# Kernel optimization log

Hardware: AMD Instinct MI355X
Metric: run time of the kernel (lower is better)

Reference implementation:

```python
import jax, jax.numpy as jnp
import numpy as np

B, D_IN, H, A, L, HEADS, C = 1024, 512, 768, 5001, 4, 2, 2
N_DATA = 56000.0
NEG = -1e30


def _gru_step(x, h, Wih, Whh, bih, bhh):
    # torch nn.GRU gate order: r, z, n
    gi = x @ Wih + bih            # [B, 3H]
    gh = h @ Whh + bhh            # [B, 3H]
    i_r, i_z, i_n = jnp.split(gi, 3, axis=-1)
    h_r, h_z, h_n = jnp.split(gh, 3, axis=-1)
    r = jax.nn.sigmoid(i_r + h_r)
    z = jax.nn.sigmoid(i_z + h_z)
    n = jnp.tanh(i_n + r * h_n)
    return (1.0 - z) * n + z * h


def _atom_selector(cls, mask, Wih, Whh, bih, bhh, hW, hb, ae_w, key):
    # cls: [B, H]; mask: [B, A] int32 (mutable copy); dropout in eval mode (identity)
    h = jnp.zeros_like(cls)
    cur_in = cls
    ae_const = jax.lax.stop_gradient(ae_w)
    probs = []
    max_index = None
    rows = jnp.arange(B)
    for j in range(L):
        h = _gru_step(cur_in, h, Wih, Whh, bih, bhh)
        logits = h @ hW + hb                      # [B, A]
        if j == 0:
            col0 = jnp.where(mask.sum(axis=-1) == 0, 1, mask[:, 0])
            mask = mask.at[:, 0].set(col0)
        else:
            mask = jnp.where((max_index == 0)[:, None], 0, mask)
            mask = mask.at[:, 0].set(1)
        masked = jnp.where(mask > 0, logits, NEG)
        u = jax.random.uniform(jax.random.fold_in(key, j), (B, A), minval=1e-9, maxval=1.0)
        g = -jnp.log(-jnp.log(u))
        y_soft = jax.nn.softmax(masked + g, axis=-1)  # tau = 1
        ind = jnp.argmax(y_soft, axis=-1)             # [B]
        y_hard = jax.nn.one_hot(ind, A, dtype=y_soft.dtype)
        prob = y_hard + y_soft - jax.lax.stop_gradient(y_soft)  # straight-through
        mask = mask.at[rows, ind].set(0)              # scatter-zero chosen atoms
        probs.append(prob)
        max_index = ind
        cur_in = cls + prob @ ae_const                # atom embedding feedback
    return jnp.stack(probs, axis=1)                   # [B, L, A]


def reference(x, x_mask, W1, b1, W2, b2, W3, b3, gru_Wih, gru_Whh, gru_bih, gru_bhh,
              head_W, head_b, ae_w, ce_Wmu, ce_bmu, ce_Wcov, ce_bcov, alpha):
    # linear_base MLP
    h = jax.nn.relu(x @ W1 + b1)
    h = jax.nn.relu(h @ W2 + b2)
    h = h @ W3 + b3                                   # cls embedding [B, H]
    key = jax.random.key(42)
    atom_probs, cps = [], []
    for i in range(HEADS):
        ap = _atom_selector(h, x_mask, gru_Wih[i], gru_Whh[i], gru_bih[i], gru_bhh[i],
                            head_W[i], head_b[i], ae_w, jax.random.fold_in(key, i))
        atom_probs.append(ap)
        # consequent estimator stand-in: mu [B,C], coverage [B]
        pooled = ap.mean(axis=1)                      # [B, A]
        mu = jax.nn.sigmoid(pooled @ ce_Wmu + ce_bmu)
        coverage = jax.nn.sigmoid(pooled @ ce_Wcov + ce_bcov)
        n = coverage * N_DATA
        sf = (alpha[0] / n)[:, None]                  # [B, 1] -> broadcast to [B, C]
        cp = (mu + sf) / (1.0 + 2.0 * sf)
        cps.append(cp)
    mat_cp = jnp.stack(cps, axis=1)                   # [B, HEADS, C]
    out = jnp.log(mat_cp.mean(axis=1))                # [B, C]
    return out, jnp.stack(atom_probs, axis=1), mat_cp


def setup_inputs() -> dict:
    key = jax.random.key(0)
    ks = jax.random.split(key, 16)
    s = 0.02
    nrm = lambda k, sh: jax.random.normal(k, sh, dtype=jnp.float32) * s
    return {
        'x': jax.random.normal(ks[0], (B, D_IN), dtype=jnp.float32),
        'x_mask': jax.random.randint(ks[1], (B, A), 0, 2, dtype=jnp.int32),
        'W1': nrm(ks[2], (D_IN, H)), 'b1': jnp.zeros((H,), jnp.float32),
        'W2': nrm(ks[3], (H, H)), 'b2': jnp.zeros((H,), jnp.float32),
        'W3': nrm(ks[4], (H, H)), 'b3': jnp.zeros((H,), jnp.float32),
        'gru_Wih': nrm(ks[5], (HEADS, H, 3 * H)), 'gru_Whh': nrm(ks[6], (HEADS, H, 3 * H)),
        'gru_bih': jnp.zeros((HEADS, 3 * H), jnp.float32), 'gru_bhh': jnp.zeros((HEADS, 3 * H), jnp.float32),
        'head_W': nrm(ks[7], (HEADS, H, A)), 'head_b': jnp.zeros((HEADS, A), jnp.float32),
        'ae_w': nrm(ks[8], (A, H)),
        'ce_Wmu': nrm(ks[9], (A, C)), 'ce_bmu': jnp.zeros((C,), jnp.float32),
        'ce_Wcov': nrm(ks[10], (A,)), 'ce_bcov': jnp.zeros((), jnp.float32),
        'alpha': jnp.ones((1,), jnp.float32),
    }
```

## Files before the change

kernel.cpp:

```cpp
#include <hip/hip_runtime.h>
#include <hip/hip_bf16.h>
#include <stdint.h>
#include <stddef.h>

#define B_DIM   1024
#define DIN     512
#define H_DIM   768
#define A_DIM   5001
#define NHEADS  2
#define NSTEPS  4
#define C_DIM   2
#define NEG_VAL -1e30f
#define BH      (B_DIM * H_DIM)

typedef unsigned short u16;
typedef __attribute__((ext_vector_type(8))) short v8s;
typedef __attribute__((ext_vector_type(4))) float v4f;

typedef const __attribute__((address_space(1))) uint32_t* gas_ptr;
typedef __attribute__((address_space(3))) uint32_t* las_ptr;

__device__ __forceinline__ void load_lds16(const void* g, void* l) {
  __builtin_amdgcn_global_load_lds((gas_ptr)g, (las_ptr)l, 16, 0, 0);
}

__host__ __device__ inline uint32_t rotl32(uint32_t x, int d) {
  return (x << d) | (x >> (32 - d));
}

__host__ __device__ inline void threefry2x32(uint32_t k0, uint32_t k1,
                                             uint32_t x0, uint32_t x1,
                                             uint32_t& o0, uint32_t& o1) {
  uint32_t ks2 = k0 ^ k1 ^ 0x1BD11BDAu;
  x0 += k0; x1 += k1;
#define TFR(d) { x0 += x1; x1 = rotl32(x1, (d)); x1 ^= x0; }
  TFR(13) TFR(15) TFR(26) TFR(6)  x0 += k1;  x1 += ks2 + 1u;
  TFR(17) TFR(29) TFR(16) TFR(24) x0 += ks2; x1 += k0 + 2u;
  TFR(13) TFR(15) TFR(26) TFR(6)  x0 += k0;  x1 += k1 + 3u;
  TFR(17) TFR(29) TFR(16) TFR(24) x0 += k1;  x1 += ks2 + 4u;
  TFR(13) TFR(15) TFR(26) TFR(6)  x0 += ks2; x1 += k0 + 5u;
#undef TFR
  o0 = x0; o1 = x1;
}

__device__ inline float gumbel_noise(uint32_t k0, uint32_t k1, uint32_t idx) {
  uint32_t o0, o1;
  threefry2x32(k0, k1, 0u, idx, o0, o1);
  uint32_t bits = o0 ^ o1;
  float f = __uint_as_float(0x3f800000u | (bits >> 9)) - 1.0f;
  float u = fmaxf(1e-9f, f * (1.0f - 1e-9f) + 1e-9f);
  return -logf(-logf(u));
}

__device__ inline float sigmoidf_(float x) { return 0.5f * tanhf(0.5f * x) + 0.5f; }

__device__ inline void split_bf16(float x, u16& hi, u16& lo) {
  __hip_bfloat16 h = __float2bfloat16(x);
  float hf = __bfloat162float(h);
  __hip_bfloat16 l = __float2bfloat16(x - hf);
  hi = *(const u16*)&h;
  lo = *(const u16*)&l;
}

__global__ __launch_bounds__(256) void split_kernel(
    const float* __restrict__ in, u16* __restrict__ hi, u16* __restrict__ lo, int n) {
  int idx = blockIdx.x * blockDim.x + threadIdx.x;
  if (idx >= n) return;
  u16 h, l;
  split_bf16(in[idx], h, l);
  hi[idx] = h; lo[idx] = l;
}

__global__ __launch_bounds__(256) void transpose_split(
    const float* __restrict__ W, u16* __restrict__ hi, u16* __restrict__ lo,
    int K, int N, size_t inStride, size_t outStride) {
  const int e = blockIdx.z;
  const float* Win = W + (size_t)e * inStride;
  u16* ho = hi + (size_t)e * outStride;
  u16* loo = lo + (size_t)e * outStride;
  __shared__ float tile[32][33];
  const int k0 = blockIdx.y * 32, n0 = blockIdx.x * 32;
  const int tx = threadIdx.x & 31, ty = threadIdx.x >> 5;
#pragma unroll
  for (int r = ty; r < 32; r += 8) {
    int n = n0 + tx;
    tile[r][tx] = (n < N) ? Win[(size_t)(k0 + r) * N + n] : 0.0f;
  }
  __syncthreads();
#pragma unroll
  for (int r = ty; r < 32; r += 8) {
    int n = n0 + r, k = k0 + tx;
    if (n < N) {
      u16 h, l;
      split_bf16(tile[tx][r], h, l);
      ho[(size_t)n * K + k] = h;
      loo[(size_t)n * K + k] = l;
    }
  }
}

struct GemmS {
  const u16* Ah[4]; const u16* Al[4];
  const u16* Bh[4]; const u16* Bl[4];
  const float* bias[4]; float* C[4];
  u16* Ch[4]; u16* Cl[4];
};

__global__ __launch_bounds__(256, 2) void gemm_mfma(
    GemmS gs, int K, int N, int Nclamp, long long ldc, int nbx, int nby, int act) {
  const int e = blockIdx.y;
  const int nwg = nbx * nby;
  const int chunk = nwg >> 3;
  const int orig = blockIdx.x;
  const int lid = (orig & 7) * chunk + (orig >> 3);
  const int by = lid % nby;
  const int bx = lid / nby;
  const int bm = by * 128, bn = bx * 128;

  __shared__ __align__(16) u16 lds[4][128 * 32];

  const int tid = threadIdx.x;
  const int wv = tid >> 6, ln = tid & 63;
  const int wr = wv >> 1, wc = wv & 1;
  const int lk = ln >> 4;
  const int lm = ln & 15;
  const int fswz = (lm >> 1) & 3;

  const int lrow = ln >> 2;
  const int slot = (ln & 3) ^ ((lrow >> 1) & 3);
  const u16* tsrc = (wv == 0) ? gs.Ah[e] : (wv == 1) ? gs.Al[e]
                  : (wv == 2) ? gs.Bh[e] : gs.Bl[e];
  const int isB = (wv >= 2);
  const int rowbase = isB ? bn : bm;

  const float* bias = gs.bias[e];

  v4f acc[4][4];
#pragma unroll
  for (int i = 0; i < 4; ++i)
#pragma unroll
    for (int j = 0; j < 4; ++j) acc[i][j] = (v4f){0.f, 0.f, 0.f, 0.f};

  for (int k0 = 0; k0 < K; k0 += 32) {
#pragma unroll
    for (int i = 0; i < 8; ++i) {
      int gr = rowbase + i * 16 + lrow;
      if (isB && gr >= Nclamp) gr = Nclamp - 1;
      const u16* gp = tsrc + (size_t)gr * K + k0 + slot * 8;
      load_lds16(gp, (void*)&lds[wv][i * 512]);
    }
    __syncthreads();

    v8s ah[4], al[4], bh[4], bl[4];
#pragma unroll
    for (int mi = 0; mi < 4; ++mi) {
      const int r = wr * 64 + mi * 16 + lm;
      const int off = r * 32 + ((lk ^ fswz) * 8);
      ah[mi] = *(const v8s*)&lds[0][off];
      al[mi] = *(const v8s*)&lds[1][off];
    }
#pragma unroll
    for (int ni = 0; ni < 4; ++ni) {
      const int r = wc * 64 + ni * 16 + lm;
      const int off = r * 32 + ((lk ^ fswz) * 8);
      bh[ni] = *(const v8s*)&lds[2][off];
      bl[ni] = *(const v8s*)&lds[3][off];
    }
#pragma unroll
    for (int mi = 0; mi < 4; ++mi)
#pragma unroll
      for (int ni = 0; ni < 4; ++ni)
        acc[mi][ni] = __builtin_amdgcn_mfma_f32_16x16x32_bf16(ah[mi], bh[ni], acc[mi][ni], 0, 0, 0);
#pragma unroll
    for (int mi = 0; mi < 4; ++mi)
#pragma unroll
      for (int ni = 0; ni < 4; ++ni)
        acc[mi][ni] = __builtin_amdgcn_mfma_f32_16x16x32_bf16(ah[mi], bl[ni], acc[mi][ni], 0, 0, 0);
#pragma unroll
    for (int mi = 0; mi < 4; ++mi)
#pragma unroll
      for (int ni = 0; ni < 4; ++ni)
        acc[mi][ni] = __builtin_amdgcn_mfma_f32_16x16x32_bf16(al[mi], bh[ni], acc[mi][ni], 0, 0, 0);

    __syncthreads();
  }

  if (gs.Ch[e]) {
    u16* ch = gs.Ch[e]; u16* cl = gs.Cl[e];
#pragma unroll
    for (int mi = 0; mi < 4; ++mi) {
      const int m = bm + wr * 64 + mi * 16 + lk * 4;
#pragma unroll
      for (int ni = 0; ni < 4; ++ni) {
        const int n = bn + wc * 64 + ni * 16 + lm;
        if (n < N) {
          const float bv = bias[n];
#pragma unroll
          for (int r = 0; r < 4; ++r) {
            float v = acc[mi][ni][r] + bv;
            if (act) v = fmaxf(v, 0.0f);
            u16 hh, ll;
            split_bf16(v, hh, ll);
            ch[(size_t)(m + r) * ldc + n] = hh;
            cl[(size_t)(m + r) * ldc + n] = ll;
          }
        }
      }
    }
  } else {
    float* C = gs.C[e];
#pragma unroll
    for (int mi = 0; mi < 4; ++mi) {
      const int m = bm + wr * 64 + mi * 16 + lk * 4;
#pragma unroll
      for (int ni = 0; ni < 4; ++ni) {
        const int n = bn + wc * 64 + ni * 16 + lm;
        if (n < N) {
          const float bv = bias[n];
          float* cp = C + (size_t)m * ldc + n;
#pragma unroll
          for (int r = 0; r < 4; ++r) {
            float v = acc[mi][ni][r] + bv;
            if (act) v = fmaxf(v, 0.0f);
            cp[(size_t)r * ldc] = v;
          }
        }
      }
    }
  }
}

__global__ __launch_bounds__(256) void init_state_kernel(
    const float* __restrict__ cls,
    u16* __restrict__ cur_hi, u16* __restrict__ cur_lo) {
  int idx = blockIdx.x * blockDim.x + threadIdx.x;
  if (idx >= 2 * BH) return;
  int rem = idx % BH;
  u16 h, l;
  split_bf16(cls[rem], h, l);
  cur_hi[idx] = h; cur_lo[idx] = l;
}

__global__ __launch_bounds__(256) void gru_combine_first(
    const float* __restrict__ gi2, const float* __restrict__ gbhh, float* __restrict__ h2,
    u16* __restrict__ h_hi, u16* __restrict__ h_lo) {
  int idx = blockIdx.x * blockDim.x + threadIdx.x;
  if (idx >= 2 * BH) return;
  int e = idx / BH, rem = idx % BH;
  int b = rem / H_DIM, c = rem - b * H_DIM;
  const float* gib = gi2 + ((size_t)e * B_DIM + b) * 3 * H_DIM;
  const float* bb = gbhh + (size_t)e * 3 * H_DIM;
  float ir = gib[c], iz = gib[H_DIM + c], inn = gib[2 * H_DIM + c];
  float hr = bb[c], hz = bb[H_DIM + c], hn = bb[2 * H_DIM + c];
  float r = sigmoidf_(ir + hr);
  float z = sigmoidf_(iz + hz);
  float n = tanhf(inn + r * hn);
  float hv = (1.0f - z) * n + z * 0.0f;
  h2[idx] = hv;
  u16 h, l;
  split_bf16(hv, h, l);
  h_hi[idx] = h; h_lo[idx] = l;
}

__global__ __launch_bounds__(256) void gru_combine_kernel(
    const float* __restrict__ gi2, const float* __restrict__ gh2, float* __restrict__ h2,
    u16* __restrict__ h_hi, u16* __restrict__ h_lo) {
  int idx = blockIdx.x * blockDim.x + threadIdx.x;
  if (idx >= 2 * BH) return;
  int e = idx / BH, rem = idx % BH;
  int b = rem / H_DIM, c = rem - b * H_DIM;
  const float* gib = gi2 + ((size_t)e * B_DIM + b) * 3 * H_DIM;
  const float* ghb = gh2 + ((size_t)e * B_DIM + b) * 3 * H_DIM;
  float ir = gib[c], iz = gib[H_DIM + c], inn = gib[2 * H_DIM + c];
  float hr = ghb[c], hz = ghb[H_DIM + c], hn = ghb[2 * H_DIM + c];
  float r = sigmoidf_(ir + hr);
  float z = sigmoidf_(iz + hz);
  float n = tanhf(inn + r * hn);
  float hv = (1.0f - z) * n + z * h2[idx];
  h2[idx] = hv;
  u16 h, l;
  split_bf16(hv, h, l);
  h_hi[idx] = h; h_lo[idx] = l;
}

#define STH 256
#define PER_TH 20

__global__ __launch_bounds__(STH) void sample_kernel(
    float* __restrict__ probs, const int* __restrict__ x_mask,
    int* __restrict__ indb, int j, uint4 keys,
    const float* __restrict__ cls, const float* __restrict__ ae_w,
    u16* __restrict__ cur_hi, u16* __restrict__ cur_lo, int docur) {
  int b = blockIdx.x;
  int e = blockIdx.y;
  int t = threadIdx.x;
  uint32_t k0 = (e == 0) ? keys.x : keys.z;
  uint32_t k1 = (e == 0) ? keys.y : keys.w;
  __shared__ float rv[STH];
  __shared__ int ri[STH];
  __shared__ int s_ind;

  float* prow = probs + (((size_t)b * NHEADS + e) * NSTEPS + j) * A_DIM;
  const int* mrow = x_mask + (size_t)b * A_DIM;

  int prev[3];
  bool dead = false;
  for (int tt = 0; tt < j; ++tt) {
    prev[tt] = indb[(e * NSTEPS + tt) * B_DIM + b];
    if (prev[tt] == 0) dead = true;
  }

  bool rowany = true;
  if (j == 0) {
    int any = 0;
    for (int a = t; a < A_DIM; a += STH) any |= mrow[a];
    ri[t] = any; __syncthreads();
    for (int s = STH / 2; s > 0; s >>= 1) {
      if (t < s) ri[t] |= ri[t + s];
      __syncthreads();
    }
    rowany = (ri[0] != 0);
    __syncthreads();
  }

  float v[PER_TH];
  float lmax = -3.0e38f;
#pragma unroll
  for (int s = 0; s < PER_TH; ++s) {
    int a = t + s * STH;
    float val = -3.0e38f;
    if (a < A_DIM) {
      int m;
      if (j == 0) {
        m = (a == 0) ? (rowany ? mrow[0] : 1) : mrow[a];
      } else if (a == 0) {
        m = 1;
      } else if (dead) {
        m = 0;
      } else {
        m = mrow[a];
        if (m) {
          for (int tt = 0; tt < j; ++tt)
            if (prev[tt] == a) { m = 0; break; }
        }
      }
      if (m > 0)
        val = prow[a] + gumbel_noise(k0, k1, (uint32_t)(b * A_DIM + a));
    }
    v[s] = val;
    lmax = fmaxf(lmax, val);
  }

  rv[t] = lmax; __syncthreads();
  for (int s = STH / 2; s > 0; s >>= 1) {
    if (t < s) rv[t] = fmaxf(rv[t], rv[t + s]);
    __syncthreads();
  }
  float m = rv[0]; __syncthreads();

  float lsum = 0.0f;
#pragma unroll
  for (int s = 0; s < PER_TH; ++s) {
    int a = t + s * STH;
    float ev = (a < A_DIM && v[s] > -1.0e37f) ? expf(v[s] - m) : 0.0f;
    v[s] = ev; lsum += ev;
  }
  rv[t] = lsum; __syncthreads();
  for (int s = STH / 2; s > 0; s >>= 1) {
    if (t < s) rv[t] += rv[t + s];
    __syncthreads();
  }
  float ssum = rv[0]; __syncthreads();

  float besty = -1.0f; int besti = A_DIM;
#pragma unroll
  for (int s = 0; s < PER_TH; ++s) {
    int a = t + s * STH;
    if (a < A_DIM) {
      float y = v[s] / ssum;
      if (y > besty) { besty = y; besti = a; }
    }
  }
  rv[t] = besty; ri[t] = besti; __syncthreads();
  for (int s = STH / 2; s > 0; s >>= 1) {
    if (t < s) {
      float y2 = rv[t + s]; int i2 = ri[t + s];
      if (y2 > rv[t] || (y2 == rv[t] && i2 < ri[t])) { rv[t] = y2; ri[t] = i2; }
    }
    __syncthreads();
  }
  if (t == 0) { s_ind = ri[0]; indb[(e * NSTEPS + j) * B_DIM + b] = ri[0]; }
  __syncthreads();
  int ind = s_ind;

  for (int a = t; a < A_DIM; a += STH) prow[a] = (a == ind) ? 1.0f : 0.0f;

  if (docur) {
    const float* crow = cls + (size_t)b * H_DIM;
    const float* arow = ae_w + (size_t)ind * H_DIM;
    u16* chh = cur_hi + (size_t)e * BH + (size_t)b * H_DIM;
    u16* cll = cur_lo + (size_t)e * BH + (size_t)b * H_DIM;
    for (int c = t; c < H_DIM; c += STH) {
      float vv = crow[c] + arow[c];
      u16 hh, ll;
      split_bf16(vv, hh, ll);
      chh[c] = hh; cll[c] = ll;
    }
  }
}

__global__ __launch_bounds__(256) void head_final_kernel(
    const int* __restrict__ indb, const float* __restrict__ Wmu,
    const float* __restrict__ bmu, const float* __restrict__ Wcov,
    const float* __restrict__ bcov, const float* __restrict__ alpha,
    float* __restrict__ matcp) {
  int idx = blockIdx.x * blockDim.x + threadIdx.x;
  if (idx >= NHEADS * B_DIM) return;
  int e = idx / B_DIM, b = idx - e * B_DIM;
  float a0 = 0.0f, a1 = 0.0f, ac = 0.0f;
  for (int j = 0; j < NSTEPS; ++j) {
    int ind = indb[(e * NSTEPS + j) * B_DIM + b];
    a0 += 0.25f * Wmu[(size_t)ind * C_DIM + 0];
    a1 += 0.25f * Wmu[(size_t)ind * C_DIM + 1];
    ac += 0.25f * Wcov[ind];
  }
  float mu0 = sigmoidf_(a0 + bmu[0]);
  float mu1 = sigmoidf_(a1 + bmu[1]);
  float cov = sigmoidf_(ac + bcov[0]);
  float n = cov * 56000.0f;
  float sf = alpha[0] / n;
  float denom = 1.0f + 2.0f * sf;
  matcp[((size_t)b * NHEADS + e) * C_DIM + 0] = (mu0 + sf) / denom;
  matcp[((size_t)b * NHEADS + e) * C_DIM + 1] = (mu1 + sf) / denom;
}

__global__ __launch_bounds__(256) void final_out_kernel(
    const float* __restrict__ matcp, float* __restrict__ out) {
  int idx = blockIdx.x * blockDim.x + threadIdx.x;
  if (idx >= B_DIM * C_DIM) return;
  int b = idx / C_DIM, c = idx - b * C_DIM;
  float s = matcp[((size_t)b * NHEADS + 0) * C_DIM + c] +
            matcp[((size_t)b * NHEADS + 1) * C_DIM + c];
  out[idx] = logf(s * 0.5f);
}

extern "C" void kernel_launch(void* const* d_in, const int* in_sizes, int n_in,
                              void* d_out, int out_size, void* d_ws, size_t ws_size,
                              hipStream_t stream) {
  const float* x     = (const float*)d_in[0];
  const int*   xmask = (const int*)d_in[1];
  const float* W1 = (const float*)d_in[2];  const float* b1 = (const float*)d_in[3];
  const float* W2 = (const float*)d_in[4];  const float* b2 = (const float*)d_in[5];
  const float* W3 = (const float*)d_in[6];  const float* b3 = (const float*)d_in[7];
  const float* gWih = (const float*)d_in[8];  const float* gWhh = (const float*)d_in[9];
  const float* gbih = (const float*)d_in[10]; const float* gbhh = (const float*)d_in[11];
  const float* hW = (const float*)d_in[12];   const float* hb = (const float*)d_in[13];
  const float* ae_w = (const float*)d_in[14];
  const float* Wmu  = (const float*)d_in[15]; const float* bmu  = (const float*)d_in[16];
  const float* Wcov = (const float*)d_in[17]; const float* bcov = (const float*)d_in[18];
  const float* alpha = (const float*)d_in[19];

  float* out = (float*)d_out;
  float* probs = out + (size_t)B_DIM * C_DIM;
  float* matcp = probs + (size_t)B_DIM * NHEADS * NSTEPS * A_DIM;

  const int HG = 3 * H_DIM;
  uint8_t* wsp = (uint8_t*)d_ws;
  auto alloc = [&](size_t bytes) {
    uint8_t* p = wsp;
    wsp += (bytes + 255) & ~(size_t)255;
    return p;
  };
  float* cls  = (float*)alloc((size_t)BH * 4);
  float* h2   = (float*)alloc((size_t)2 * BH * 4);
  float* gi2  = (float*)alloc((size_t)2 * B_DIM * HG * 4);
  float* gh2  = (float*)alloc((size_t)2 * B_DIM * HG * 4);
  u16* h_hi   = (u16*)alloc((size_t)2 * BH * 2);
  u16* h_lo   = (u16*)alloc((size_t)2 * BH * 2);
  u16* cur_hi = (u16*)alloc((size_t)2 * BH * 2);
  u16* cur_lo = (u16*)alloc((size_t)2 * BH * 2);
  u16* WihT_h = (u16*)alloc((size_t)2 * HG * H_DIM * 2);
  u16* WihT_l = (u16*)alloc((size_t)2 * HG * H_DIM * 2);
  u16* WhhT_h = (u16*)alloc((size_t)2 * HG * H_DIM * 2);
  u16* WhhT_l = (u16*)alloc((size_t)2 * HG * H_DIM * 2);
  u16* hWT_h  = (u16*)alloc((size_t)2 * A_DIM * H_DIM * 2);
  u16* hWT_l  = (u16*)alloc((size_t)2 * A_DIM * H_DIM * 2);
  u16* x_hi   = (u16*)alloc((size_t)B_DIM * DIN * 2);
  u16* x_lo   = (u16*)alloc((size_t)B_DIM * DIN * 2);
  u16* t1_hi  = (u16*)alloc((size_t)BH * 2);
  u16* t1_lo  = (u16*)alloc((size_t)BH * 2);
  u16* t2_hi  = (u16*)alloc((size_t)BH * 2);
  u16* t2_lo  = (u16*)alloc((size_t)BH * 2);
  u16* W1T_h  = (u16*)alloc((size_t)H_DIM * DIN * 2);
  u16* W1T_l  = (u16*)alloc((size_t)H_DIM * DIN * 2);
  u16* W2T_h  = (u16*)alloc((size_t)H_DIM * H_DIM * 2);
  u16* W2T_l  = (u16*)alloc((size_t)H_DIM * H_DIM * 2);
  u16* W3T_h  = (u16*)alloc((size_t)H_DIM * H_DIM * 2);
  u16* W3T_l  = (u16*)alloc((size_t)H_DIM * H_DIM * 2);
  int* indb   = (int*)alloc((size_t)NHEADS * NSTEPS * B_DIM * 4);

  dim3 blk(256);

  transpose_split<<<dim3(HG / 32, H_DIM / 32, 2), blk, 0, stream>>>(
      gWih, WihT_h, WihT_l, H_DIM, HG, (size_t)H_DIM * HG, (size_t)HG * H_DIM);
  transpose_split<<<dim3(HG / 32, H_DIM / 32, 2), blk, 0, stream>>>(
      gWhh, WhhT_h, WhhT_l, H_DIM, HG, (size_t)H_DIM * HG, (size_t)HG * H_DIM);
  transpose_split<<<dim3((A_DIM + 31) / 32, H_DIM / 32, 2), blk, 0, stream>>>(
      hW, hWT_h, hWT_l, H_DIM, A_DIM, (size_t)H_DIM * A_DIM, (size_t)A_DIM * H_DIM);
  transpose_split<<<dim3(H_DIM / 32, DIN / 32, 1), blk, 0, stream>>>(
      W1, W1T_h, W1T_l, DIN, H_DIM, 0, 0);
  transpose_split<<<dim3(H_DIM / 32, H_DIM / 32, 1), blk, 0, stream>>>(
      W2, W2T_h, W2T_l, H_DIM, H_DIM, 0, 0);
  transpose_split<<<dim3(H_DIM / 32, H_DIM / 32, 1), blk, 0, stream>>>(
      W3, W3T_h, W3T_l, H_DIM, H_DIM, 0, 0);
  split_kernel<<<(B_DIM * DIN + 255) / 256, blk, 0, stream>>>(x, x_hi, x_lo, B_DIM * DIN);

  {
    GemmS g{};
    g.Ah[0] = x_hi; g.Al[0] = x_lo; g.Bh[0] = W1T_h; g.Bl[0] = W1T_l;
    g.bias[0] = b1; g.C[0] = nullptr; g.Ch[0] = t1_hi; g.Cl[0] = t1_lo;
    gemm_mfma<<<dim3((H_DIM / 128) * (B_DIM / 128), 1), blk, 0, stream>>>(
        g, DIN, H_DIM, H_DIM, (long long)H_DIM, H_DIM / 128, B_DIM / 128, 1);
  }
  {
    GemmS g{};
    g.Ah[0] = t1_hi; g.Al[0] = t1_lo; g.Bh[0] = W2T_h; g.Bl[0] = W2T_l;
    g.bias[0] = b2; g.C[0] = nullptr; g.Ch[0] = t2_hi; g.Cl[0] = t2_lo;
    gemm_mfma<<<dim3((H_DIM / 128) * (B_DIM / 128), 1), blk, 0, stream>>>(
        g, H_DIM, H_DIM, H_DIM, (long long)H_DIM, H_DIM / 128, B_DIM / 128, 1);
  }
  {
    GemmS g{};
    g.Ah[0] = t2_hi; g.Al[0] = t2_lo; g.Bh[0] = W3T_h; g.Bl[0] = W3T_l;
    g.bias[0] = b3; g.C[0] = cls; g.Ch[0] = nullptr;
    gemm_mfma<<<dim3((H_DIM / 128) * (B_DIM / 128), 1), blk, 0, stream>>>(
        g, H_DIM, H_DIM, H_DIM, (long long)H_DIM, H_DIM / 128, B_DIM / 128, 0);
  }

  init_state_kernel<<<(2 * BH + 255) / 256, blk, 0, stream>>>(cls, cur_hi, cur_lo);

  uint32_t bk0 = 0u, bk1 = 42u;
  uint32_t hk[2][2];
  threefry2x32(bk0, bk1, 0u, 0u, hk[0][0], hk[0][1]);
  threefry2x32(bk0, bk1, 0u, 1u, hk[1][0], hk[1][1]);

  for (int j = 0; j < NSTEPS; ++j) {
    if (j == 0) {
      GemmS gb{};
      for (int head = 0; head < NHEADS; ++head) {
        gb.Ah[head] = cur_hi + (size_t)head * BH;
        gb.Al[head] = cur_lo + (size_t)head * BH;
        gb.Bh[head] = WihT_h + (size_t)head * HG * H_DIM;
        gb.Bl[head] = WihT_l + (size_t)head * HG * H_DIM;
        gb.bias[head] = gbih + (size_t)head * HG;
        gb.C[head] = gi2 + (size_t)head * B_DIM * HG;
      }
      gemm_mfma<<<dim3((HG / 128) * (B_DIM / 128), 2), blk, 0, stream>>>(
          gb, H_DIM, HG, HG, (long long)HG, HG / 128, B_DIM / 128, 0);
      gru_combine_first<<<(2 * BH + 255) / 256, blk, 0, stream>>>(gi2, gbhh, h2, h_hi, h_lo);
    } else {
      GemmS gb{};
      for (int head = 0; head < NHEADS; ++head) {
        gb.Ah[head * 2 + 0] = cur_hi + (size_t)head * BH;
        gb.Al[head * 2 + 0] = cur_lo + (size_t)head * BH;
        gb.Bh[head * 2 + 0] = WihT_h + (size_t)head * HG * H_DIM;
        gb.Bl[head * 2 + 0] = WihT_l + (size_t)head * HG * H_DIM;
        gb.bias[head * 2 + 0] = gbih + (size_t)head * HG;
        gb.C[head * 2 + 0] = gi2 + (size_t)head * B_DIM * HG;
        gb.Ah[head * 2 + 1] = h_hi + (size_t)head * BH;
        gb.Al[head * 2 + 1] = h_lo + (size_t)head * BH;
        gb.Bh[head * 2 + 1] = WhhT_h + (size_t)head * HG * H_DIM;
        gb.Bl[head * 2 + 1] = WhhT_l + (size_t)head * HG * H_DIM;
        gb.bias[head * 2 + 1] = gbhh + (size_t)head * HG;
        gb.C[head * 2 + 1] = gh2 + (size_t)head * B_DIM * HG;
      }
      gemm_mfma<<<dim3((HG / 128) * (B_DIM / 128), 4), blk, 0, stream>>>(
          gb, H_DIM, HG, HG, (long long)HG, HG / 128, B_DIM / 128, 0);
      gru_combine_kernel<<<(2 * BH + 255) / 256, blk, 0, stream>>>(gi2, gh2, h2, h_hi, h_lo);
    }

    GemmS lb{};
    for (int head = 0; head < NHEADS; ++head) {
      lb.Ah[head] = h_hi + (size_t)head * BH;
      lb.Al[head] = h_lo + (size_t)head * BH;
      lb.Bh[head] = hWT_h + (size_t)head * A_DIM * H_DIM;
      lb.Bl[head] = hWT_l + (size_t)head * A_DIM * H_DIM;
      lb.bias[head] = hb + (size_t)head * A_DIM;
      lb.C[head] = probs + (size_t)(head * NSTEPS + j) * A_DIM;
    }
    gemm_mfma<<<dim3(40 * (B_DIM / 128), 2), blk, 0, stream>>>(
        lb, H_DIM, A_DIM, A_DIM, (long long)NHEADS * NSTEPS * A_DIM, 40, B_DIM / 128, 0);

    uint32_t s00, s01, s10, s11;
    threefry2x32(hk[0][0], hk[0][1], 0u, (uint32_t)j, s00, s01);
    threefry2x32(hk[1][0], hk[1][1], 0u, (uint32_t)j, s10, s11);
    uint4 keys; keys.x = s00; keys.y = s01; keys.z = s10; keys.w = s11;
    sample_kernel<<<dim3(B_DIM, NHEADS), dim3(STH), 0, stream>>>(
        probs, xmask, indb, j, keys, cls, ae_w, cur_hi, cur_lo, (j < NSTEPS - 1) ? 1 : 0);
  }

  head_final_kernel<<<(NHEADS * B_DIM + 255) / 256, blk, 0, stream>>>(
      indb, Wmu, bmu, Wcov, bcov, alpha, matcp);
  final_out_kernel<<<(B_DIM * C_DIM + 255) / 256, blk, 0, stream>>>(matcp, out);
}
```

Measured before the change: 838.7 us.

## Batch weight transposes, deepen GEMM K-tile, fuse Whh GEMM into logits launch

Merges the nine weight transpose-split launches into one batched kernel and folds the cls split/duplication into the W3 GEMM epilogue, which removes init_state_kernel. The GEMM K-step doubles from 32 to 64 with a new XOR swizzle, and LDS use grows to 64 KB per block, which may limit occupancy. The next step's h@Whh GEMM is moved into the same launch as the logits GEMM, using per-entry N/nbx so that early-exiting blocks handle the mixed grid sizes. The aim is fewer launches and better overlap of the small GRU GEMM with the large head GEMM.

```diff
diff --git a/kernel.cpp b/kernel.cpp
--- a/kernel.cpp
+++ b/kernel.cpp
@@ -71,30 +71,29 @@
   hi[idx] = h; lo[idx] = l;
 }
 
-__global__ __launch_bounds__(256) void transpose_split(
-    const float* __restrict__ W, u16* __restrict__ hi, u16* __restrict__ lo,
-    int K, int N, size_t inStride, size_t outStride) {
-  const int e = blockIdx.z;
-  const float* Win = W + (size_t)e * inStride;
-  u16* ho = hi + (size_t)e * outStride;
-  u16* loo = lo + (size_t)e * outStride;
+struct TS { const float* W; u16* hi; u16* lo; int K; int N; };
+struct TS9 { TS t[9]; };
+
+__global__ __launch_bounds__(256) void transpose_split_b(TS9 ts) {
+  const TS p = ts.t[blockIdx.z];
+  const int k0 = blockIdx.y * 32, n0 = blockIdx.x * 32;
+  if (k0 >= p.K || n0 >= p.N) return;
   __shared__ float tile[32][33];
-  const int k0 = blockIdx.y * 32, n0 = blockIdx.x * 32;
   const int tx = threadIdx.x & 31, ty = threadIdx.x >> 5;
 #pragma unroll
   for (int r = ty; r < 32; r += 8) {
     int n = n0 + tx;
-    tile[r][tx] = (n < N) ? Win[(size_t)(k0 + r) * N + n] : 0.0f;
+    tile[r][tx] = (n < p.N) ? p.W[(size_t)(k0 + r) * p.N + n] : 0.0f;
   }
   __syncthreads();
 #pragma unroll
   for (int r = ty; r < 32; r += 8) {
     int n = n0 + r, k = k0 + tx;
-    if (n < N) {
+    if (n < p.N) {
       u16 h, l;
       split_bf16(tile[tx][r], h, l);
-      ho[(size_t)n * K + k] = h;
-      loo[(size_t)n * K + k] = l;
+      p.hi[(size_t)n * p.K + k] = h;
+      p.lo[(size_t)n * p.K + k] = l;
     }
   }
 }
@@ -102,143 +101,121 @@
 struct GemmS {
   const u16* Ah[4]; const u16* Al[4];
   const u16* Bh[4]; const u16* Bl[4];
-  const float* bias[4]; float* C[4];
+  const float* bias[4];
+  float* C[4];
   u16* Ch[4]; u16* Cl[4];
+  int N[4]; int nbx[4]; long long ldc[4]; int act[4]; int dup[4];
 };
 
-__global__ __launch_bounds__(256, 2) void gemm_mfma(
-    GemmS gs, int K, int N, int Nclamp, long long ldc, int nbx, int nby, int act) {
+__global__ __launch_bounds__(256, 2) void gemm_mfma(GemmS gs, int K, int nby) {
   const int e = blockIdx.y;
-  const int nwg = nbx * nby;
+  const int nwg = gridDim.x;
   const int chunk = nwg >> 3;
-  const int orig = blockIdx.x;
-  const int lid = (orig & 7) * chunk + (orig >> 3);
+  const int lid = (blockIdx.x & 7) * chunk + (blockIdx.x >> 3);
   const int by = lid % nby;
   const int bx = lid / nby;
+  if (bx >= gs.nbx[e]) return;
   const int bm = by * 128, bn = bx * 128;
-
-  __shared__ __align__(16) u16 lds[4][128 * 32];
+  const int N = gs.N[e];
+
+  __shared__ __align__(16) u16 lds[4][128 * 64];
 
   const int tid = threadIdx.x;
   const int wv = tid >> 6, ln = tid & 63;
   const int wr = wv >> 1, wc = wv & 1;
   const int lk = ln >> 4;
   const int lm = ln & 15;
-  const int fswz = (lm >> 1) & 3;
-
-  const int lrow = ln >> 2;
-  const int slot = (ln & 3) ^ ((lrow >> 1) & 3);
+
+  const int lrow8 = ln >> 3;
+  const int sslot = (ln & 7) ^ lrow8;
   const u16* tsrc = (wv == 0) ? gs.Ah[e] : (wv == 1) ? gs.Al[e]
                   : (wv == 2) ? gs.Bh[e] : gs.Bl[e];
   const int isB = (wv >= 2);
   const int rowbase = isB ? bn : bm;
 
+  v4f acc[4][4];
+#pragma unroll
+  for (int i = 0; i < 4; ++i)
+#pragma unroll
+    for (int j = 0; j < 4; ++j) acc[i][j] = (v4f){0.f, 0.f, 0.f, 0.f};
+
+  for (int k0 = 0; k0 < K; k0 += 64) {
+#pragma unroll
+    for (int i = 0; i < 16; ++i) {
+      int gr = rowbase + i * 8 + lrow8;
+      if (isB && gr >= N) gr = N - 1;
+      const u16* gp = tsrc + (size_t)gr * K + k0 + sslot * 8;
+      load_lds16(gp, (void*)&lds[wv][i * 512]);
+    }
+    __syncthreads();
+
+#pragma unroll
+    for (int kh = 0; kh < 2; ++kh) {
+      v8s ah[4], al[4], bh[4], bl[4];
+#pragma unroll
+      for (int mi = 0; mi < 4; ++mi) {
+        const int r = wr * 64 + mi * 16 + lm;
+        const int off = r * 64 + (((kh * 4 + lk) ^ (r & 7)) * 8);
+        ah[mi] = *(const v8s*)&lds[0][off];
+        al[mi] = *(const v8s*)&lds[1][off];
+      }
+#pragma unroll
+      for (int ni = 0; ni < 4; ++ni) {
+        const int r = wc * 64 + ni * 16 + lm;
+        const int off = r * 64 + (((kh * 4 + lk) ^ (r & 7)) * 8);
+        bh[ni] = *(const v8s*)&lds[2][off];
+        bl[ni] = *(const v8s*)&lds[3][off];
+      }
+#pragma unroll
+      for (int mi = 0; mi < 4; ++mi)
+#pragma unroll
+        for (int ni = 0; ni < 4; ++ni)
+          acc[mi][ni] = __builtin_amdgcn_mfma_f32_16x16x32_bf16(ah[mi], bh[ni], acc[mi][ni], 0, 0, 0);
+#pragma unroll
+      for (int mi = 0; mi < 4; ++mi)
+#pragma unroll
+        for (int ni = 0; ni < 4; ++ni)
+          acc[mi][ni] = __builtin_amdgcn_mfma_f32_16x16x32_bf16(ah[mi], bl[ni], acc[mi][ni], 0, 0, 0);
+#pragma unroll
+      for (int mi = 0; mi < 4; ++mi)
+#pragma unroll
+        for (int ni = 0; ni < 4; ++ni)
+          acc[mi][ni] = __builtin_amdgcn_mfma_f32_16x16x32_bf16(al[mi], bh[ni], acc[mi][ni], 0, 0, 0);
+    }
+
+    __syncthreads();
+  }
+
   const float* bias = gs.bias[e];
-
-  v4f acc[4][4];
-#pragma unroll
-  for (int i = 0; i < 4; ++i)
-#pragma unroll
-    for (int j = 0; j < 4; ++j) acc[i][j] = (v4f){0.f, 0.f, 0.f, 0.f};
-
-  for (int k0 = 0; k0 < K; k0 += 32) {
-#pragma unroll
-    for (int i = 0; i < 8; ++i) {
-      int gr = rowbase + i * 16 + lrow;
-      if (isB && gr >= Nclamp) gr = Nclamp - 1;
-      const u16* gp = tsrc + (size_t)gr * K + k0 + slot * 8;
-      load_lds16(gp, (void*)&lds[wv][i * 512]);
-    }
-    __syncthreads();
-
-    v8s ah[4], al[4], bh[4], bl[4];
-#pragma unroll
-    for (int mi = 0; mi < 4; ++mi) {
-      const int r = wr * 64 + mi * 16 + lm;
-      const int off = r * 32 + ((lk ^ fswz) * 8);
-      ah[mi] = *(const v8s*)&lds[0][off];
-      al[mi] = *(const v8s*)&lds[1][off];
-    }
+  const long long ldc = gs.ldc[e];
+  const int act = gs.act[e];
+  float* Cf = gs.C[e];
+  u16* ch = gs.Ch[e]; u16* cl = gs.Cl[e];
+  const int dup = gs.dup[e];
+#pragma unroll
+  for (int mi = 0; mi < 4; ++mi) {
+    const int m = bm + wr * 64 + mi * 16 + lk * 4;
 #pragma unroll
     for (int ni = 0; ni < 4; ++ni) {
-      const int r = wc * 64 + ni * 16 + lm;
-      const int off = r * 32 + ((lk ^ fswz) * 8);
-      bh[ni] = *(const v8s*)&lds[2][off];
-      bl[ni] = *(const v8s*)&lds[3][off];
-    }
-#pragma unroll
-    for (int mi = 0; mi < 4; ++mi)
-#pragma unroll
-      for (int ni = 0; ni < 4; ++ni)
-        acc[mi][ni] = __builtin_amdgcn_mfma_f32_16x16x32_bf16(ah[mi], bh[ni], acc[mi][ni], 0, 0, 0);
-#pragma unroll
-    for (int mi = 0; mi < 4; ++mi)
-#pragma unroll
-      for (int ni = 0; ni < 4; ++ni)
-        acc[mi][ni] = __builtin_amdgcn_mfma_f32_16x16x32_bf16(ah[mi], bl[ni], acc[mi][ni], 0, 0, 0);
-#pragma unroll
-    for (int mi = 0; mi < 4; ++mi)
-#pragma unroll
-      for (int ni = 0; ni < 4; ++ni)
-        acc[mi][ni] = __builtin_amdgcn_mfma_f32_16x16x32_bf16(al[mi], bh[ni], acc[mi][ni], 0, 0, 0);
-
-    __syncthreads();
-  }
-
-  if (gs.Ch[e]) {
-    u16* ch = gs.Ch[e]; u16* cl = gs.Cl[e];
-#pragma unroll
-    for (int mi = 0; mi < 4; ++mi) {
-      const int m = bm + wr * 64 + mi * 16 + lk * 4;
-#pragma unroll
-      for (int ni = 0; ni < 4; ++ni) {
-        const int n = bn + wc * 64 + ni * 16 + lm;
-        if (n < N) {
-          const float bv = bias[n];
-#pragma unroll
-          for (int r = 0; r < 4; ++r) {
-            float v = acc[mi][ni][r] + bv;
-            if (act) v = fmaxf(v, 0.0f);
+      const int n = bn + wc * 64 + ni * 16 + lm;
+      if (n < N) {
+        const float bv = bias[n];
+#pragma unroll
+        for (int r = 0; r < 4; ++r) {
+          float v = acc[mi][ni][r] + bv;
+          if (act) v = fmaxf(v, 0.0f);
+          const size_t ix = (size_t)(m + r) * ldc + n;
+          if (Cf) Cf[ix] = v;
+          if (ch) {
             u16 hh, ll;
             split_bf16(v, hh, ll);
-            ch[(size_t)(m + r) * ldc + n] = hh;
-            cl[(size_t)(m + r) * ldc + n] = ll;
+            ch[ix] = hh; cl[ix] = ll;
+            if (dup) { ch[ix + (size_t)BH] = hh; cl[ix + (size_t)BH] = ll; }
           }
         }
       }
     }
-  } else {
-    float* C = gs.C[e];
-#pragma unroll
-    for (int mi = 0; mi < 4; ++mi) {
-      const int m = bm + wr * 64 + mi * 16 + lk * 4;
-#pragma unroll
-      for (int ni = 0; ni < 4; ++ni) {
-        const int n = bn + wc * 64 + ni * 16 + lm;
-        if (n < N) {
-          const float bv = bias[n];
-          float* cp = C + (size_t)m * ldc + n;
-#pragma unroll
-          for (int r = 0; r < 4; ++r) {
-            float v = acc[mi][ni][r] + bv;
-            if (act) v = fmaxf(v, 0.0f);
-            cp[(size_t)r * ldc] = v;
-          }
-        }
-      }
-    }
-  }
-}
-
-__global__ __launch_bounds__(256) void init_state_kernel(
-    const float* __restrict__ cls,
-    u16* __restrict__ cur_hi, u16* __restrict__ cur_lo) {
-  int idx = blockIdx.x * blockDim.x + threadIdx.x;
-  if (idx >= 2 * BH) return;
-  int rem = idx % BH;
-  u16 h, l;
-  split_bf16(cls[rem], h, l);
-  cur_hi[idx] = h; cur_lo[idx] = l;
+  }
 }
 
 __global__ __launch_bounds__(256) void gru_combine_first(
@@ -501,95 +478,87 @@
 
   dim3 blk(256);
 
-  transpose_split<<<dim3(HG / 32, H_DIM / 32, 2), blk, 0, stream>>>(
-      gWih, WihT_h, WihT_l, H_DIM, HG, (size_t)H_DIM * HG, (size_t)HG * H_DIM);
-  transpose_split<<<dim3(HG / 32, H_DIM / 32, 2), blk, 0, stream>>>(
-      gWhh, WhhT_h, WhhT_l, H_DIM, HG, (size_t)H_DIM * HG, (size_t)HG * H_DIM);
-  transpose_split<<<dim3((A_DIM + 31) / 32, H_DIM / 32, 2), blk, 0, stream>>>(
-      hW, hWT_h, hWT_l, H_DIM, A_DIM, (size_t)H_DIM * A_DIM, (size_t)A_DIM * H_DIM);
-  transpose_split<<<dim3(H_DIM / 32, DIN / 32, 1), blk, 0, stream>>>(
-      W1, W1T_h, W1T_l, DIN, H_DIM, 0, 0);
-  transpose_split<<<dim3(H_DIM / 32, H_DIM / 32, 1), blk, 0, stream>>>(
-      W2, W2T_h, W2T_l, H_DIM, H_DIM, 0, 0);
-  transpose_split<<<dim3(H_DIM / 32, H_DIM / 32, 1), blk, 0, stream>>>(
-      W3, W3T_h, W3T_l, H_DIM, H_DIM, 0, 0);
+  {
+    TS9 ts;
+    ts.t[0] = {gWih,                    WihT_h,                    WihT_l,                    H_DIM, HG};
+    ts.t[1] = {gWih + (size_t)H_DIM*HG, WihT_h + (size_t)HG*H_DIM, WihT_l + (size_t)HG*H_DIM, H_DIM, HG};
+    ts.t[2] = {gWhh,                    WhhT_h,                    WhhT_l,                    H_DIM, HG};
+    ts.t[3] = {gWhh + (size_t)H_DIM*HG, WhhT_h + (size_t)HG*H_DIM, WhhT_l + (size_t)HG*H_DIM, H_DIM, HG};
+    ts.t[4] = {hW,                          hWT_h,                           hWT_l,                           H_DIM, A_DIM};
+    ts.t[5] = {hW + (size_t)H_DIM*A_DIM,    hWT_h + (size_t)A_DIM*H_DIM,     hWT_l + (size_t)A_DIM*H_DIM,     H_DIM, A_DIM};
+    ts.t[6] = {W1, W1T_h, W1T_l, DIN,   H_DIM};
+    ts.t[7] = {W2, W2T_h, W2T_l, H_DIM, H_DIM};
+    ts.t[8] = {W3, W3T_h, W3T_l, H_DIM, H_DIM};
+    transpose_split_b<<<dim3((A_DIM + 31) / 32, H_DIM / 32, 9), blk, 0, stream>>>(ts);
+  }
   split_kernel<<<(B_DIM * DIN + 255) / 256, blk, 0, stream>>>(x, x_hi, x_lo, B_DIM * DIN);
+
+  auto setE = [](GemmS& g, int e, const u16* ah, const u16* al, const u16* bhp, const u16* blp,
+                 const float* bias, float* Cf, u16* chp, u16* clp,
+                 int N, int nbx, long long ldc, int act, int dup) {
+    g.Ah[e] = ah; g.Al[e] = al; g.Bh[e] = bhp; g.Bl[e] = blp;
+    g.bias[e] = bias; g.C[e] = Cf; g.Ch[e] = chp; g.Cl[e] = clp;
+    g.N[e] = N; g.nbx[e] = nbx; g.ldc[e] = ldc; g.act[e] = act; g.dup[e] = dup;
+  };
 
   {
     GemmS g{};
-    g.Ah[0] = x_hi; g.Al[0] = x_lo; g.Bh[0] = W1T_h; g.Bl[0] = W1T_l;
-    g.bias[0] = b1; g.C[0] = nullptr; g.Ch[0] = t1_hi; g.Cl[0] = t1_lo;
-    gemm_mfma<<<dim3((H_DIM / 128) * (B_DIM / 128), 1), blk, 0, stream>>>(
-        g, DIN, H_DIM, H_DIM, (long long)H_DIM, H_DIM / 128, B_DIM / 128, 1);
+    setE(g, 0, x_hi, x_lo, W1T_h, W1T_l, b1, nullptr, t1_hi, t1_lo, H_DIM, H_DIM / 128, H_DIM, 1, 0);
+    gemm_mfma<<<dim3((H_DIM / 128) * 8, 1), blk, 0, stream>>>(g, DIN, 8);
   }
   {
     GemmS g{};
-    g.Ah[0] = t1_hi; g.Al[0] = t1_lo; g.Bh[0] = W2T_h; g.Bl[0] = W2T_l;
-    g.bias[0] = b2; g.C[0] = nullptr; g.Ch[0] = t2_hi; g.Cl[0] = t2_lo;
-    gemm_mfma<<<dim3((H_DIM / 128) * (B_DIM / 128), 1), blk, 0, stream>>>(
-        g, H_DIM, H_DIM, H_DIM, (long long)H_DIM, H_DIM / 128, B_DIM / 128, 1);
+    setE(g, 0, t1_hi, t1_lo, W2T_h, W2T_l, b2, nullptr, t2_hi, t2_lo, H_DIM, H_DIM / 128, H_DIM, 1, 0);
+    gemm_mfma<<<dim3((H_DIM / 128) * 8, 1), blk, 0, stream>>>(g, H_DIM, 8);
   }
   {
     GemmS g{};
-    g.Ah[0] = t2_hi; g.Al[0] = t2_lo; g.Bh[0] = W3T_h; g.Bl[0] = W3T_l;
-    g.bias[0] = b3; g.C[0] = cls; g.Ch[0] = nullptr;
-    gemm_mfma<<<dim3((H_DIM / 128) * (B_DIM / 128), 1), blk, 0, stream>>>(
-        g, H_DIM, H_DIM, H_DIM, (long long)H_DIM, H_DIM / 128, B_DIM / 128, 0);
-  }
-
-  init_state_kernel<<<(2 * BH + 255) / 256, blk, 0, stream>>>(cls, cur_hi, cur_lo);
+    setE(g, 0, t2_hi, t2_lo, W3T_h, W3T_l, b3, cls, cur_hi, cur_lo, H_DIM, H_DIM / 128, H_DIM, 0, 1);
+    gemm_mfma<<<dim3((H_DIM / 128) * 8, 1), blk, 0, stream>>>(g, H_DIM, 8);
+  }
 
   uint32_t bk0 = 0u, bk1 = 42u;
   uint32_t hk[2][2];
   threefry2x32(bk0, bk1, 0u, 0u, hk[0][0], hk[0][1]);
   threefry2x32(bk0, bk1, 0u, 1u, hk[1][0], hk[1][1]);
 
+  const int NBX_L = (A_DIM + 127) / 128;
+  const int NBX_G = HG / 128;
+
   for (int j = 0; j < NSTEPS; ++j) {
-    if (j == 0) {
-      GemmS gb{};
-      for (int head = 0; head < NHEADS; ++head) {
-        gb.Ah[head] = cur_hi + (size_t)head * BH;
-        gb.Al[head] = cur_lo + (size_t)head * BH;
-        gb.Bh[head] = WihT_h + (size_t)head * HG * H_DIM;
-        gb.Bl[head] = WihT_l + (size_t)head * HG * H_DIM;
-        gb.bias[head] = gbih + (size_t)head * HG;
-        gb.C[head] = gi2 + (size_t)head * B_DIM * HG;
+    {
+      GemmS g{};
+      for (int head = 0; head < NHEADS; ++head)
+        setE(g, head, cur_hi + (size_t)head * BH, cur_lo + (size_t)head * BH,
+             WihT_h + (size_t)head * HG * H_DIM, WihT_l + (size_t)head * HG * H_DIM,
+             gbih + (size_t)head * HG, gi2 + (size_t)head * B_DIM * HG, nullptr, nullptr,
+             HG, NBX_G, HG, 0, 0);
+      gemm_mfma<<<dim3(NBX_G * 8, 2), blk, 0, stream>>>(g, H_DIM, 8);
+    }
+
+    if (j == 0)
+      gru_combine_first<<<(2 * BH + 255) / 256, blk, 0, stream>>>(gi2, gbhh, h2, h_hi, h_lo);
+    else
+      gru_combine_kernel<<<(2 * BH + 255) / 256, blk, 0, stream>>>(gi2, gh2, h2, h_hi, h_lo);
+
+    {
+      GemmS g{};
+      for (int head = 0; head < NHEADS; ++head)
+        setE(g, head, h_hi + (size_t)head * BH, h_lo + (size_t)head * BH,
+             hWT_h + (size_t)head * A_DIM * H_DIM, hWT_l + (size_t)head * A_DIM * H_DIM,
+             hb + (size_t)head * A_DIM, probs + (size_t)(head * NSTEPS + j) * A_DIM,
+             nullptr, nullptr, A_DIM, NBX_L, (long long)NHEADS * NSTEPS * A_DIM, 0, 0);
+      if (j < NSTEPS - 1) {
+        for (int head = 0; head < NHEADS; ++head)
+          setE(g, 2 + head, h_hi + (size_t)head * BH, h_lo + (size_t)head * BH,
+               WhhT_h + (size_t)head * HG * H_DIM, WhhT_l + (size_t)head * HG * H_DIM,
+               gbhh + (size_t)head * HG, gh2 + (size_t)head * B_DIM * HG, nullptr, nullptr,
+               HG, NBX_G, HG, 0, 0);
+        gemm_mfma<<<dim3(NBX_L * 8, 4), blk, 0, stream>>>(g, H_DIM, 8);
+      } else {
+        gemm_mfma<<<dim3(NBX_L * 8, 2), blk, 0, stream>>>(g, H_DIM, 8);
       }
-      gemm_mfma<<<dim3((HG / 128) * (B_DIM / 128), 2), blk, 0, stream>>>(
-          gb, H_DIM, HG, HG, (long long)HG, HG / 128, B_DIM / 128, 0);
-      gru_combine_first<<<(2 * BH + 255) / 256, blk, 0, stream>>>(gi2, gbhh, h2, h_hi, h_lo);
-    } else {
-      GemmS gb{};
-      for (int head = 0; head < NHEADS; ++head) {
-        gb.Ah[head * 2 + 0] = cur_hi + (size_t)head * BH;
-        gb.Al[head * 2 + 0] = cur_lo + (size_t)head * BH;
-        gb.Bh[head * 2 + 0] = WihT_h + (size_t)head * HG * H_DIM;
-        gb.Bl[head * 2 + 0] = WihT_l + (size_t)head * HG * H_DIM;
-        gb.bias[head * 2 + 0] = gbih + (size_t)head * HG;
-        gb.C[head * 2 + 0] = gi2 + (size_t)head * B_DIM * HG;
-        gb.Ah[head * 2 + 1] = h_hi + (size_t)head * BH;
-        gb.Al[head * 2 + 1] = h_lo + (size_t)head * BH;
-        gb.Bh[head * 2 + 1] = WhhT_h + (size_t)head * HG * H_DIM;
-        gb.Bl[head * 2 + 1] = WhhT_l + (size_t)head * HG * H_DIM;
-        gb.bias[head * 2 + 1] = gbhh + (size_t)head * HG;
-        gb.C[head * 2 + 1] = gh2 + (size_t)head * B_DIM * HG;
-      }
-      gemm_mfma<<<dim3((HG / 128) * (B_DIM / 128), 4), blk, 0, stream>>>(
-          gb, H_DIM, HG, HG, (long long)HG, HG / 128, B_DIM / 128, 0);
-      gru_combine_kernel<<<(2 * BH + 255) / 256, blk, 0, stream>>>(gi2, gh2, h2, h_hi, h_lo);
-    }
-
-    GemmS lb{};
-    for (int head = 0; head < NHEADS; ++head) {
-      lb.Ah[head] = h_hi + (size_t)head * BH;
-      lb.Al[head] = h_lo + (size_t)head * BH;
-      lb.Bh[head] = hWT_h + (size_t)head * A_DIM * H_DIM;
-      lb.Bl[head] = hWT_l + (size_t)head * A_DIM * H_DIM;
-      lb.bias[head] = hb + (size_t)head * A_DIM;
-      lb.C[head] = probs + (size_t)(head * NSTEPS + j) * A_DIM;
-    }
-    gemm_mfma<<<dim3(40 * (B_DIM / 128), 2), blk, 0, stream>>>(
-        lb, H_DIM, A_DIM, A_DIM, (long long)NHEADS * NSTEPS * A_DIM, 40, B_DIM / 128, 0);
+    }
 
     uint32_t s00, s01, s10, s11;
     threefry2x32(hk[0][0], hk[0][1], 0u, (uint32_t)j, s00, s01);
```

Result: slower. 870.8 us (+3.8%).
